# Kernel optimization log

Measured on AMD Instinct MI355X. Metric: run time of the kernel, lower is better.

## Reference

```python
import jax, jax.numpy as jnp
import numpy as np

KERNEL_DIMS = 16
BOND = 4
OUT = 10
STEP = KERNEL_DIMS // 4          # 4
D = STEP * STEP                  # in_dims = 16
BATCH = 128


def setup_inputs() -> dict:
    key = jax.random.key(0)
    ks = jax.random.split(key, 9)
    d, b = D, BOND
    inp = {
        "inputs": jax.random.normal(ks[0], (BATCH, KERNEL_DIMS, KERNEL_DIMS, 1), dtype=jnp.float32),
        # entanglers (stddev 1e-4 as in the original init)
        "e1": jax.random.normal(ks[1], (d, d, d, d, b, b, b, b), dtype=jnp.float32) * 1e-4,
        "e2": jax.random.normal(ks[2], (b, b, b, b, b, b, b, b), dtype=jnp.float32) * 1e-4,
        # isometries (stddev 1e-5), leg orders exactly as in the source
        "iso1_0": jax.random.normal(ks[3], (d, d, d, b, b), dtype=jnp.float32) * 1e-5,
        "iso1_1": jax.random.normal(ks[4], (d, d, b, d, b), dtype=jnp.float32) * 1e-5,
        "iso1_2": jax.random.normal(ks[5], (d, b, d, d, b), dtype=jnp.float32) * 1e-5,
        "iso1_3": jax.random.normal(ks[6], (b, d, d, d, b), dtype=jnp.float32) * 1e-5,
        "iso2": jax.random.normal(ks[7], (b, b, b, b, OUT), dtype=jnp.float32) * 1e-5,
        "bias": jnp.zeros((OUT,), dtype=jnp.float32),
    }
    return inp


def reference(inputs, e1, e2, iso1_0, iso1_1, iso1_2, iso1_3, iso2, bias):
    B = inputs.shape[0]
    # 4x4 grid of step x step patches, each flattened to D features.
    # patch index k = i*4 + ii, matching the python loops in the original.
    xv = (inputs[..., 0]
          .reshape(B, 4, STEP, 4, STEP)
          .transpose(0, 1, 3, 2, 4)
          .reshape(B, 16, D))           # [B, 16, D]
    p = lambda k: xv[:, k, :]

    # entangler 1: legs 0-3 contract with patches 5,6,9,10; legs 4-7 go to isometries.
    v = jnp.einsum('abcdefgh,Ba,Bb,Bc,Bd->Befgh', e1, p(5), p(6), p(9), p(10))  # [B,b,b,b,b]

    # layer-1 isometries: contract their three patch legs, keep (bond-in m, bond-out o).
    t0 = jnp.einsum('ijkmo,Bi,Bj,Bk->Bmo', iso1_0, p(0), p(1), p(4))    # m = e1 leg4
    t1 = jnp.einsum('ijmko,Bi,Bj,Bk->Bmo', iso1_1, p(2), p(3), p(7))    # m = e1 leg5
    t2 = jnp.einsum('imjko,Bi,Bj,Bk->Bmo', iso1_2, p(8), p(12), p(13))  # m = e1 leg6
    t3 = jnp.einsum('mijko,Bi,Bj,Bk->Bmo', iso1_3, p(11), p(14), p(15)) # m = e1 leg7

    # fuse entangler-1 output with the four isometry bond maps -> entangler-2 inputs.
    w = jnp.einsum('Befgh,Bea,Bfb,Bgc,Bhd->Babcd', v, t0, t1, t2, t3)   # [B,b,b,b,b]

    # entangler 2 then top isometry into output_dims.
    out = jnp.einsum('Babcd,abcdefgh,efghC->BC', w, e2, iso2)           # [B, OUT]
    return out + bias
```

## Files before the change

### kernel.cpp

```cpp
#include <hip/hip_runtime.h>


#define KC 64

typedef __attribute__((ext_vector_type(8))) short bf16x8;
typedef __attribute__((ext_vector_type(4))) float f32x4;

__device__ __forceinline__ int poff(int p, int d) {
    return ((p >> 2) * 4 + (d >> 2)) * 16 + (p & 3) * 4 + (d & 3);
}

__device__ __forceinline__ void splitf(float x, short& h, short& l) {
    unsigned u = __builtin_bit_cast(unsigned, x);
    h = (short)(u >> 16);
    float hf = __builtin_bit_cast(float, u & 0xFFFF0000u);
    float rem = x - hf;
    l = (short)(__builtin_bit_cast(unsigned, rem) >> 16);
}

__global__ void __launch_bounds__(256) k2_iso(
        const float* __restrict__ i0, const float* __restrict__ i1,
        const float* __restrict__ i2, const float* __restrict__ i3,
        const float* __restrict__ in, float* __restrict__ tt) {
    int b = blockIdx.x, iso = blockIdx.y;
    int t = threadIdx.x;

    const int pid0[4] = {0, 2, 8, 11};
    const int pid1[4] = {1, 3, 12, 14};
    const int pid2[4] = {4, 7, 13, 15};
    const int siA[4] = {4096, 4096, 4096, 1024};
    const int sjA[4] = {256, 256, 64, 64};
    const int skA[4] = {16, 4, 4, 4};
    const int smA[4] = {4, 64, 1024, 16384};

    const float* iso_p = (iso == 0) ? i0 : (iso == 1) ? i1 : (iso == 2) ? i2 : i3;

    __shared__ float pX[16], pY[16], pZ[16];
    if (t < 16)      pX[t]      = in[b * 256 + poff(pid0[iso], t)];
    else if (t < 32) pY[t - 16] = in[b * 256 + poff(pid1[iso], t - 16)];
    else if (t < 48) pZ[t - 32] = in[b * 256 + poff(pid2[iso], t - 32)];
    __syncthreads();

    int i = t >> 4, j = t & 15;
    float pxy = pX[i] * pY[j];
    int sk = skA[iso], sm = smA[iso];
    const float* basep = iso_p + i * siA[iso] + j * sjA[iso];

    float acc[16];
#pragma unroll
    for (int mo = 0; mo < 16; ++mo) acc[mo] = 0.f;

    for (int k = 0; k < 16; ++k) {
        float w = pxy * pZ[k];
        const float* kp = basep + k * sk;
#pragma unroll
        for (int m = 0; m < 4; ++m) {
            float4 v = *(const float4*)(kp + m * sm);
            acc[m * 4 + 0] += w * v.x;
            acc[m * 4 + 1] += w * v.y;
            acc[m * 4 + 2] += w * v.z;
            acc[m * 4 + 3] += w * v.w;
        }
    }

    __shared__ float red[16 * 257];
    __shared__ float part[256];
#pragma unroll
    for (int mo = 0; mo < 16; ++mo) red[mo * 257 + t] = acc[mo];
    __syncthreads();
    int mo = t & 15, seg = t >> 4;
    float s = 0.f;
#pragma unroll
    for (int u = 0; u < 16; ++u) s += red[mo * 257 + seg * 16 + u];
    part[mo * 16 + seg] = s;
    __syncthreads();
    if (t < 16) {
        float o = 0.f;
#pragma unroll
        for (int s2 = 0; s2 < 16; ++s2) o += part[t * 16 + s2];
        tt[iso * 2048 + b * 16 + t] = o;
    }
}

__global__ void k3_m2(const float* __restrict__ e2, const float* __restrict__ iso2,
                      float* __restrict__ M2) {
    __shared__ float is2[2560];
    int t = threadIdx.x;
    for (int s = t; s < 2560; s += 256) is2[s] = iso2[s];
    __syncthreads();
    int flat = blockIdx.x * 256 + t;
    int q = flat / 10, C = flat % 10;
    float acc = 0.f;
    for (int r = 0; r < 256; ++r) acc += e2[q * 256 + r] * is2[r * 10 + C];
    M2[q * 10 + C] = acc;
}

__global__ void __launch_bounds__(512, 4) k4_mfma(const float* __restrict__ e1,
                                                  const float* __restrict__ in,
                                                  float* __restrict__ vpart) {
    int kc = blockIdx.x;
    int ny = blockIdx.y;
    int tid = threadIdx.x;
    int wv = tid >> 6;
    int lane = tid & 63;
    int l15 = lane & 15;
    int g = lane >> 4;
    int d0 = (g & 1) * 8;
    bool hic = (g & 2) != 0;

    int b = wv * 16 + l15;
    const float* xb = in + b * 256;

    float p9r[16], p10r[8], p5r;
#pragma unroll
    for (int c = 0; c < 16; ++c) p9r[c] = xb[128 + (c >> 2) * 16 + 4 + (c & 3)];
#pragma unroll
    for (int j = 0; j < 8; ++j) {
        int d = d0 + j;
        p10r[j] = xb[128 + (d >> 2) * 16 + 8 + (d & 3)];
    }
    {
        int a = kc >> 2;
        p5r = xb[64 + (a >> 2) * 16 + 4 + (a & 3)];
    }

    int colbase = ny * 32;
    int col0 = colbase + l15;

    f32x4 acc[2];
#pragma unroll
    for (int tn = 0; tn < 2; ++tn) acc[tn] = (f32x4){0.f, 0.f, 0.f, 0.f};

    const float* ep = e1 + ((size_t)(kc * 1024 + g * 8)) * 256;

    for (int abi = 0; abi < 4; ++abi) {
        int a2 = (kc & 3) * 4 + abi;
        float sab = p5r * xb[64 + (a2 >> 2) * 16 + 8 + (a2 & 3)];
#pragma unroll
        for (int cc = 0; cc < 8; ++cc) {
            bf16x8 eh[2], el[2];
#pragma unroll
            for (int tn = 0; tn < 2; ++tn) {
                const float* ec = ep + (size_t)cc * 32 * 256 + col0 + tn * 16;
#pragma unroll
                for (int j = 0; j < 8; ++j) {
                    float evj = ec[(size_t)j * 256];
                    short h, l; splitf(evj, h, l);
                    eh[tn][j] = h; el[tn][j] = l;
                }
            }
            bf16x8 wh, wl;
            {
                float s0 = sab * p9r[2 * cc];
                float s1 = sab * p9r[2 * cc + 1];
                float s = hic ? s1 : s0;
#pragma unroll
                for (int j = 0; j < 8; ++j) {
                    float wj = s * p10r[j];
                    short h, l; splitf(wj, h, l);
                    wh[j] = h; wl[j] = l;
                }
            }
#pragma unroll
            for (int tn = 0; tn < 2; ++tn) {
                acc[tn] = __builtin_amdgcn_mfma_f32_16x16x32_bf16(wh, eh[tn], acc[tn], 0, 0, 0);
                acc[tn] = __builtin_amdgcn_mfma_f32_16x16x32_bf16(wh, el[tn], acc[tn], 0, 0, 0);
                acc[tn] = __builtin_amdgcn_mfma_f32_16x16x32_bf16(wl, eh[tn], acc[tn], 0, 0, 0);
            }
        }
        ep += (size_t)256 * 256;
    }

    int brow = wv * 16 + g * 4;
#pragma unroll
    for (int tn = 0; tn < 2; ++tn) {
        int col = colbase + tn * 16 + l15;
#pragma unroll
        for (int r = 0; r < 4; ++r) {
            vpart[((size_t)kc * 128 + brow + r) * 256 + col] = acc[tn][r];
        }
    }
}

__global__ void __launch_bounds__(256) k5_final(
        const float* __restrict__ vpart, const float* __restrict__ tt,
        const float* __restrict__ M2, const float* __restrict__ bias,
        float* __restrict__ out) {
    __shared__ float v[256], A[256], Bb[256];
    __shared__ float t0[16], t1[16], t2[16], t3[16];
    int b = blockIdx.x, t = threadIdx.x;

    float s = 0.f;
#pragma unroll 8
    for (int kc = 0; kc < KC; ++kc) {
        s += vpart[((size_t)kc * 128 + b) * 256 + t];
    }
    v[t] = s;
    if (t < 16) {
        t0[t] = tt[0 * 2048 + b * 16 + t];
        t1[t] = tt[1 * 2048 + b * 16 + t];
        t2[t] = tt[2 * 2048 + b * 16 + t];
        t3[t] = tt[3 * 2048 + b * 16 + t];
    }
    __syncthreads();

    {
        int a = t >> 6, fgh = t & 63;
        float acc = 0.f;
#pragma unroll
        for (int e = 0; e < 4; ++e) acc += t0[e * 4 + a] * v[e * 64 + fgh];
        A[t] = acc;
    }
    __syncthreads();
    {
        int a = t >> 6, bb = (t >> 4) & 3, gh = t & 15;
        float acc = 0.f;
#pragma unroll
        for (int f = 0; f < 4; ++f) acc += t1[f * 4 + bb] * A[a * 64 + f * 16 + gh];
        Bb[t] = acc;
    }
    __syncthreads();
    {
        int ab = t >> 4, c = (t >> 2) & 3, h = t & 3;
        float acc = 0.f;
#pragma unroll
        for (int g = 0; g < 4; ++g) acc += t2[g * 4 + c] * Bb[ab * 16 + g * 4 + h];
        A[t] = acc;
    }
    __syncthreads();
    {
        int abc = t >> 2, dd = t & 3;
        float acc = 0.f;
#pragma unroll
        for (int h = 0; h < 4; ++h) acc += t3[h * 4 + dd] * A[abc * 4 + h];
        Bb[t] = acc;
    }
    __syncthreads();
    if (t < 10) {
        float acc = bias[t];
        for (int q = 0; q < 256; ++q) acc += Bb[q] * M2[q * 10 + t];
        out[b * 10 + t] = acc;
    }
}

extern "C" void kernel_launch(void* const* d_in, const int* in_sizes, int n_in,
                              void* d_out, int out_size, void* d_ws, size_t ws_size,
                              hipStream_t stream) {
    const float* in    = (const float*)d_in[0];
    const float* e1    = (const float*)d_in[1];
    const float* e2    = (const float*)d_in[2];
    const float* iso10 = (const float*)d_in[3];
    const float* iso11 = (const float*)d_in[4];
    const float* iso12 = (const float*)d_in[5];
    const float* iso13 = (const float*)d_in[6];
    const float* iso2  = (const float*)d_in[7];
    const float* bias  = (const float*)d_in[8];
    float* out = (float*)d_out;

    char* ws = (char*)d_ws;
    float* tt    = (float*)(ws + 131072);
    float* M2    = (float*)(ws + 163840);
    float* vpart = (float*)(ws + 262144);

    hipLaunchKernelGGL(k2_iso, dim3(128, 4), dim3(256), 0, stream,
                       iso10, iso11, iso12, iso13, in, tt);
    hipLaunchKernelGGL(k3_m2, dim3(10), dim3(256), 0, stream, e2, iso2, M2);
    hipLaunchKernelGGL(k4_mfma, dim3(KC, 8), dim3(512), 0, stream, e1, in, vpart);
    hipLaunchKernelGGL(k5_final, dim3(128), dim3(256), 0, stream,
                       vpart, tt, M2, bias, out);
}
```

Baseline: 198.7 us.

## Retile e1 MFMA kernel so each wave covers four batch tiles, split-K finer

The e1 contraction kernel is retiled so each wave computes four 16-row batch tiles that share one set of split bf16 e1 fragments. This cuts the number of times each e1 element is loaded and split per batch row. The K dimension is split into 256 chunks instead of 64, giving more blocks to fill the GPU. The partial-sum layout becomes batch-major so the final reduction reads contiguous memory. The cost is a much larger partial buffer (32 MB) and more reduction work in the final kernel, with a fallback to 64 chunks when the workspace is too small.

```diff
diff --git a/kernel.cpp b/kernel.cpp
--- a/kernel.cpp
+++ b/kernel.cpp
@@ -1,7 +1,5 @@
 #include <hip/hip_runtime.h>
 
-
-#define KC 64
 
 typedef __attribute__((ext_vector_type(8))) short bf16x8;
 typedef __attribute__((ext_vector_type(4))) float f32x4;
@@ -95,48 +93,57 @@
     M2[q * 10 + C] = acc;
 }
 
-__global__ void __launch_bounds__(512, 4) k4_mfma(const float* __restrict__ e1,
+template<int NABI>
+__global__ void __launch_bounds__(256, 4) k4_mfma(const float* __restrict__ e1,
                                                   const float* __restrict__ in,
-                                                  float* __restrict__ vpart) {
-    int kc = blockIdx.x;
+                                                  float* __restrict__ vpart,
+                                                  int kcc_total) {
+    int bx = blockIdx.x;
     int ny = blockIdx.y;
     int tid = threadIdx.x;
     int wv = tid >> 6;
     int lane = tid & 63;
+    int mg = wv >> 1;
+    int ngr = wv & 1;
     int l15 = lane & 15;
     int g = lane >> 4;
     int d0 = (g & 1) * 8;
-    bool hic = (g & 2) != 0;
-
-    int b = wv * 16 + l15;
-    const float* xb = in + b * 256;
-
-    float p9r[16], p10r[8], p5r;
-#pragma unroll
-    for (int c = 0; c < 16; ++c) p9r[c] = xb[128 + (c >> 2) * 16 + 4 + (c & 3)];
-#pragma unroll
-    for (int j = 0; j < 8; ++j) {
-        int d = d0 + j;
-        p10r[j] = xb[128 + (d >> 2) * 16 + 8 + (d & 3)];
-    }
-    {
-        int a = kc >> 2;
-        p5r = xb[64 + (a >> 2) * 16 + 4 + (a & 3)];
-    }
-
-    int colbase = ny * 32;
+    int hic = (g & 2) ? 1 : 0;
+
+    const float* xb[4];
+#pragma unroll
+    for (int t = 0; t < 4; ++t) xb[t] = in + (mg * 64 + t * 16 + l15) * 256;
+
+    float p10r[4][8];
+#pragma unroll
+    for (int t = 0; t < 4; ++t)
+#pragma unroll
+        for (int j = 0; j < 8; ++j) {
+            int d = d0 + j;
+            p10r[t][j] = xb[t][128 + (d >> 2) * 16 + 8 + (d & 3)];
+        }
+
+    int colbase = ny * 64 + ngr * 32;
     int col0 = colbase + l15;
 
-    f32x4 acc[2];
-#pragma unroll
-    for (int tn = 0; tn < 2; ++tn) acc[tn] = (f32x4){0.f, 0.f, 0.f, 0.f};
-
-    const float* ep = e1 + ((size_t)(kc * 1024 + g * 8)) * 256;
-
-    for (int abi = 0; abi < 4; ++abi) {
-        int a2 = (kc & 3) * 4 + abi;
-        float sab = p5r * xb[64 + (a2 >> 2) * 16 + 8 + (a2 & 3)];
-#pragma unroll
+    f32x4 acc[4][2];
+#pragma unroll
+    for (int t = 0; t < 4; ++t)
+#pragma unroll
+        for (int tn = 0; tn < 2; ++tn)
+            acc[t][tn] = (f32x4){0.f, 0.f, 0.f, 0.f};
+
+    for (int ai = 0; ai < NABI; ++ai) {
+        int kcc = bx * NABI + ai;
+        int a = kcc >> 4, a2 = kcc & 15;
+        float sab[4];
+#pragma unroll
+        for (int t = 0; t < 4; ++t)
+            sab[t] = xb[t][64 + (a >> 2) * 16 + 4 + (a & 3)]
+                   * xb[t][64 + (a2 >> 2) * 16 + 8 + (a2 & 3)];
+
+        const float* ep = e1 + ((size_t)(kcc * 256 + g * 8)) * 256;
+
         for (int cc = 0; cc < 8; ++cc) {
             bf16x8 eh[2], el[2];
 #pragma unroll
@@ -144,44 +151,46 @@
                 const float* ec = ep + (size_t)cc * 32 * 256 + col0 + tn * 16;
 #pragma unroll
                 for (int j = 0; j < 8; ++j) {
-                    float evj = ec[(size_t)j * 256];
-                    short h, l; splitf(evj, h, l);
+                    short h, l; splitf(ec[(size_t)j * 256], h, l);
                     eh[tn][j] = h; el[tn][j] = l;
                 }
             }
-            bf16x8 wh, wl;
-            {
-                float s0 = sab * p9r[2 * cc];
-                float s1 = sab * p9r[2 * cc + 1];
-                float s = hic ? s1 : s0;
+            int c = 2 * cc + hic;
+            int p9off = 128 + (c >> 2) * 16 + 4 + (c & 3);
+#pragma unroll
+            for (int t = 0; t < 4; ++t) {
+                float s = sab[t] * xb[t][p9off];
+                bf16x8 wh, wl;
 #pragma unroll
                 for (int j = 0; j < 8; ++j) {
-                    float wj = s * p10r[j];
-                    short h, l; splitf(wj, h, l);
+                    short h, l; splitf(s * p10r[t][j], h, l);
                     wh[j] = h; wl[j] = l;
                 }
+#pragma unroll
+                for (int tn = 0; tn < 2; ++tn) {
+                    acc[t][tn] = __builtin_amdgcn_mfma_f32_16x16x32_bf16(wh, eh[tn], acc[t][tn], 0, 0, 0);
+                    acc[t][tn] = __builtin_amdgcn_mfma_f32_16x16x32_bf16(wh, el[tn], acc[t][tn], 0, 0, 0);
+                    acc[t][tn] = __builtin_amdgcn_mfma_f32_16x16x32_bf16(wl, eh[tn], acc[t][tn], 0, 0, 0);
+                }
             }
-#pragma unroll
-            for (int tn = 0; tn < 2; ++tn) {
-                acc[tn] = __builtin_amdgcn_mfma_f32_16x16x32_bf16(wh, eh[tn], acc[tn], 0, 0, 0);
-                acc[tn] = __builtin_amdgcn_mfma_f32_16x16x32_bf16(wh, el[tn], acc[tn], 0, 0, 0);
-                acc[tn] = __builtin_amdgcn_mfma_f32_16x16x32_bf16(wl, eh[tn], acc[tn], 0, 0, 0);
+        }
+    }
+
+#pragma unroll
+    for (int t = 0; t < 4; ++t) {
+        int brow = mg * 64 + t * 16 + g * 4;
+#pragma unroll
+        for (int tn = 0; tn < 2; ++tn) {
+            int col = colbase + tn * 16 + l15;
+#pragma unroll
+            for (int r = 0; r < 4; ++r) {
+                vpart[((size_t)(brow + r) * kcc_total + bx) * 256 + col] = acc[t][tn][r];
             }
         }
-        ep += (size_t)256 * 256;
-    }
-
-    int brow = wv * 16 + g * 4;
-#pragma unroll
-    for (int tn = 0; tn < 2; ++tn) {
-        int col = colbase + tn * 16 + l15;
-#pragma unroll
-        for (int r = 0; r < 4; ++r) {
-            vpart[((size_t)kc * 128 + brow + r) * 256 + col] = acc[tn][r];
-        }
-    }
-}
-
+    }
+}
+
+template<int KCC>
 __global__ void __launch_bounds__(256) k5_final(
         const float* __restrict__ vpart, const float* __restrict__ tt,
         const float* __restrict__ M2, const float* __restrict__ bias,
@@ -190,11 +199,10 @@
     __shared__ float t0[16], t1[16], t2[16], t3[16];
     int b = blockIdx.x, t = threadIdx.x;
 
+    const float* vp = vpart + (size_t)b * KCC * 256 + t;
     float s = 0.f;
-#pragma unroll 8
-    for (int kc = 0; kc < KC; ++kc) {
-        s += vpart[((size_t)kc * 128 + b) * 256 + t];
-    }
+#pragma unroll 16
+    for (int k = 0; k < KCC; ++k) s += vp[(size_t)k * 256];
     v[t] = s;
     if (t < 16) {
         t0[t] = tt[0 * 2048 + b * 16 + t];
@@ -265,7 +273,17 @@
     hipLaunchKernelGGL(k2_iso, dim3(128, 4), dim3(256), 0, stream,
                        iso10, iso11, iso12, iso13, in, tt);
     hipLaunchKernelGGL(k3_m2, dim3(10), dim3(256), 0, stream, e2, iso2, M2);
-    hipLaunchKernelGGL(k4_mfma, dim3(KC, 8), dim3(512), 0, stream, e1, in, vpart);
-    hipLaunchKernelGGL(k5_final, dim3(128), dim3(256), 0, stream,
-                       vpart, tt, M2, bias, out);
-}
+
+    size_t need = (size_t)262144 + (size_t)128 * 256 * 256 * 4;
+    if (ws_size >= need) {
+        hipLaunchKernelGGL(k4_mfma<1>, dim3(256, 4), dim3(256), 0, stream,
+                           e1, in, vpart, 256);
+        hipLaunchKernelGGL(k5_final<256>, dim3(128), dim3(256), 0, stream,
+                           vpart, tt, M2, bias, out);
+    } else {
+        hipLaunchKernelGGL(k4_mfma<4>, dim3(64, 4), dim3(256), 0, stream,
+                           e1, in, vpart, 64);
+        hipLaunchKernelGGL(k5_final<64>, dim3(128), dim3(256), 0, stream,
+                           vpart, tt, M2, bias, out);
+    }
+}
```

New measurement: 196.1 us. About the same (-1.3%).
